# Kernel tuning notes

Hardware: AMD Instinct MI355X
Metric: run time of the kernel (lower is better)

## Reference

```python
import jax, jax.numpy as jnp
import numpy as np
from jax import lax

NB_VERTICES = 2048  # init kwarg nb_vertices
N_POINTS = 524288


def setup_inputs() -> dict:
    key = jax.random.key(0)
    pos = jax.random.normal(key, (N_POINTS, 3), dtype=jnp.float32)
    return {"pos": pos}


def _fps_indices(pos, m):
    """Single-pass iterative farthest point sampling.
    pos: [N, 3] float. Returns int32 indices [m].
    Maintains a running min squared-distance buffer (classic FPS).
    """
    N = pos.shape[0]
    big = jnp.asarray(jnp.finfo(pos.dtype).max, pos.dtype)
    min_d = jnp.full((N,), big, dtype=pos.dtype)
    idxs = jnp.zeros((m,), dtype=jnp.int32)  # idxs[0] = 0 (deterministic start)

    def body(i, carry):
        min_d, idxs = carry
        last = jnp.take(pos, idxs[i - 1], axis=0)          # [3]
        d = jnp.sum((pos - last[None, :]) ** 2, axis=-1)    # [N]
        min_d = jnp.minimum(min_d, d)
        nxt = jnp.argmax(min_d).astype(jnp.int32)
        idxs = idxs.at[i].set(nxt)
        return (min_d, idxs)

    _, idxs = lax.fori_loop(1, m, body, (min_d, idxs))
    return idxs


@jax.jit
def _forward(pos):
    # ratio = nb_vertices / N  ->  fps returns ceil(N*ratio) = nb_vertices
    # indices in a single pass, so the original while-loop runs once.
    idxs = _fps_indices(pos, NB_VERTICES)
    return pos[idxs]  # [nb_vertices, 3]


def reference(pos):
    return _forward(pos)
```

## Files before the change

kernel.cpp:

```cpp
#include <hip/hip_runtime.h>
#include <float.h>


#define NPTS     524288
#define MOUT     2048
#define NBLK     64
#define NTHR     512
#define NWAVE    (NTHR / 64)
#define GTHREADS (NBLK * NTHR)
#define PPT      (NPTS / GTHREADS)
#define SLOT_STRIDE 8
#define MASK51   ((1ull << 51) - 1)


__global__ void __launch_bounds__(NTHR, 1) fps_kernel(
    const float* __restrict__ pos, float* __restrict__ out,
    unsigned long long* __restrict__ slots)
{
    const unsigned tid  = threadIdx.x;
    const unsigned lane = tid & 63u;
    const unsigned wav  = tid >> 6;
    const unsigned blk  = blockIdx.x;
    const unsigned g    = blk * NTHR + tid;

    float X[PPT], Y[PPT], Z[PPT], D[PPT];
#pragma unroll
    for (int p = 0; p < PPT; ++p) {
        const unsigned idx = g + (unsigned)p * GTHREADS;
        X[p] = pos[3u * idx + 0];
        Y[p] = pos[3u * idx + 1];
        Z[p] = pos[3u * idx + 2];
        D[p] = FLT_MAX;
    }

    float px = pos[0], py = pos[1], pz = pos[2];
    if (g == 0) { out[0] = px; out[1] = py; out[2] = pz; }

    __shared__ unsigned long long sred[2][NWAVE];
    __shared__ unsigned long long sbc[2][4];
    if (tid < 4) { sbc[0][tid] = 0ull; sbc[1][tid] = 0ull; }

    for (int i = 1; i < MOUT; ++i) {
        float bv = -1.0f;
        unsigned bi = 0;
#pragma unroll
        for (int p = 0; p < PPT; ++p) {
            float dx = __fsub_rn(X[p], px);
            float dy = __fsub_rn(Y[p], py);
            float dz = __fsub_rn(Z[p], pz);
            float d  = __fadd_rn(__fadd_rn(__fmul_rn(dx, dx), __fmul_rn(dy, dy)),
                                 __fmul_rn(dz, dz));
            float m  = fminf(D[p], d);
            D[p] = m;
            if (m > bv) { bv = m; bi = g + (unsigned)p * GTHREADS; }
        }
        unsigned long long best =
            ((unsigned long long)__float_as_uint(bv) << 19) |
            (unsigned long long)((NPTS - 1u) - bi);

#pragma unroll
        for (int off = 32; off > 0; off >>= 1) {
            unsigned long long o = __shfl_xor(best, off, 64);
            if (o > best) best = o;
        }

        unsigned long long* sb = sred[i & 1];
        if (lane == 0) sb[wav] = best;
        __syncthreads();

        const unsigned long long tag = (unsigned long long)i;
        const unsigned long long tb  = tag << 51;

        if (wav == 0) {
            unsigned long long b2 = sb[lane & (NWAVE - 1u)];
#pragma unroll
            for (int off = NWAVE / 2; off > 0; off >>= 1) {
                unsigned long long o = __shfl_xor(b2, off, 64);
                if (o > b2) b2 = o;
            }

            unsigned long long* buf =
                slots + (unsigned)(i & 1) * (NBLK * SLOT_STRIDE);
            if (lane == 0) {
                __hip_atomic_store(&buf[blk * SLOT_STRIDE], tb | b2,
                                   __ATOMIC_RELAXED, __HIP_MEMORY_SCOPE_AGENT);
            }

            unsigned long long s;
            do {
                s = __hip_atomic_load(&buf[lane * SLOT_STRIDE],
                                      __ATOMIC_RELAXED, __HIP_MEMORY_SCOPE_AGENT);
                if ((s >> 51) == tag) break;
                __builtin_amdgcn_s_sleep(1);
            } while (true);
            unsigned long long c = s & MASK51;

            unsigned cidx = (NPTS - 1u) - (unsigned)(c & 0x7FFFFull);
            float cx = pos[3u * cidx + 0];
            float cy = pos[3u * cidx + 1];
            float cz = pos[3u * cidx + 2];

            unsigned long long win = c;
#pragma unroll
            for (int off = 32; off > 0; off >>= 1) {
                unsigned long long o = __shfl_xor(win, off, 64);
                if (o > win) win = o;
            }
            unsigned long long bal = __ballot(win == c);
            int src = __ffsll(bal) - 1;
            px = __shfl(cx, src, 64);
            py = __shfl(cy, src, 64);
            pz = __shfl(cz, src, 64);

            if (lane < 3) {
                float cv = (lane == 0) ? px : (lane == 1) ? py : pz;
                __hip_atomic_store(&sbc[i & 1][lane],
                                   tb | (unsigned long long)__float_as_uint(cv),
                                   __ATOMIC_RELAXED, __HIP_MEMORY_SCOPE_WORKGROUP);
            }

            if (blk == 0 && lane == 0) {
                out[3 * i + 0] = px; out[3 * i + 1] = py; out[3 * i + 2] = pz;
            }
        } else {
            unsigned long long xw, yw, zw;
            do {
                xw = __hip_atomic_load(&sbc[i & 1][0],
                                       __ATOMIC_RELAXED, __HIP_MEMORY_SCOPE_WORKGROUP);
                yw = __hip_atomic_load(&sbc[i & 1][1],
                                       __ATOMIC_RELAXED, __HIP_MEMORY_SCOPE_WORKGROUP);
                zw = __hip_atomic_load(&sbc[i & 1][2],
                                       __ATOMIC_RELAXED, __HIP_MEMORY_SCOPE_WORKGROUP);
                if (((xw >> 51) == tag) & ((yw >> 51) == tag) &
                    ((zw >> 51) == tag)) break;
                __builtin_amdgcn_s_sleep(1);
            } while (true);
            px = __uint_as_float((unsigned)xw);
            py = __uint_as_float((unsigned)yw);
            pz = __uint_as_float((unsigned)zw);
        }
    }
}

extern "C" void kernel_launch(void* const* d_in, const int* in_sizes, int n_in,
                              void* d_out, int out_size, void* d_ws, size_t ws_size,
                              hipStream_t stream) {
    const float* pos = (const float*)d_in[0];
    float* out = (float*)d_out;
    unsigned long long* slots = (unsigned long long*)d_ws;

    void* args[] = { (void*)&pos, (void*)&out, (void*)&slots };
    hipLaunchCooperativeKernel((void*)fps_kernel, dim3(NBLK), dim3(NTHR),
                               args, 0, stream);
}
```

Measured before the change: 5.165 ms.

## Carry winner coordinates through reductions and use DPP wave max

Each thread now tracks the coordinates of its best point. Those coordinates travel with the wave and block reductions and are published to the global slots alongside the packed key. This removes the dependent global gather of the winning point's position after the cross-block exchange, which sits on the serial critical path of every iteration. Shuffle-based 64-bit max reductions are replaced with DPP row operations plus readlane. In exchange there are more global stores and loads per slot, extra select instructions per point, and a multi-word tag protocol that relies on relaxed-ordering visibility.

```diff
diff --git a/kernel.cpp b/kernel.cpp
--- a/kernel.cpp
+++ b/kernel.cpp
@@ -13,6 +13,44 @@
 #define MASK51   ((1ull << 51) - 1)
 
 
+#define DPP_MAX_U64(v, ctrl) do {                                            \
+    unsigned _lo = (unsigned)__builtin_amdgcn_update_dpp(                    \
+        0, (int)(unsigned)(v), (ctrl), 0xf, 0xf, true);                      \
+    unsigned _hi = (unsigned)__builtin_amdgcn_update_dpp(                    \
+        0, (int)(unsigned)((v) >> 32), (ctrl), 0xf, 0xf, true);              \
+    unsigned long long _s = ((unsigned long long)_hi << 32) | _lo;           \
+    if (_s > (v)) (v) = _s;                                                  \
+} while (0)
+
+__device__ __forceinline__ unsigned long long wave_max_u64(unsigned long long v)
+{
+    DPP_MAX_U64(v, 0x111);
+    DPP_MAX_U64(v, 0x112);
+    DPP_MAX_U64(v, 0x114);
+    DPP_MAX_U64(v, 0x118);
+    DPP_MAX_U64(v, 0x142);
+    DPP_MAX_U64(v, 0x143);
+    unsigned lo = (unsigned)__builtin_amdgcn_readlane((int)(unsigned)v, 63);
+    unsigned hi = (unsigned)__builtin_amdgcn_readlane((int)(unsigned)(v >> 32), 63);
+    return ((unsigned long long)hi << 32) | lo;
+}
+
+__device__ __forceinline__ unsigned long long oct_max_u64(unsigned long long v)
+{
+    DPP_MAX_U64(v, 0x111);
+    DPP_MAX_U64(v, 0x112);
+    DPP_MAX_U64(v, 0x114);
+    unsigned lo = (unsigned)__builtin_amdgcn_readlane((int)(unsigned)v, 7);
+    unsigned hi = (unsigned)__builtin_amdgcn_readlane((int)(unsigned)(v >> 32), 7);
+    return ((unsigned long long)hi << 32) | lo;
+}
+
+__device__ __forceinline__ float readlane_f(float v, int l)
+{
+    return __uint_as_float(
+        (unsigned)__builtin_amdgcn_readlane((int)__float_as_uint(v), l));
+}
+
 __global__ void __launch_bounds__(NTHR, 1) fps_kernel(
     const float* __restrict__ pos, float* __restrict__ out,
     unsigned long long* __restrict__ slots)
@@ -37,6 +75,7 @@
     if (g == 0) { out[0] = px; out[1] = py; out[2] = pz; }
 
     __shared__ unsigned long long sred[2][NWAVE];
+    __shared__ float scx[2][NWAVE], scy[2][NWAVE], scz[2][NWAVE];
     __shared__ unsigned long long sbc[2][4];
     if (tid < 4) { sbc[0][tid] = 0ull; sbc[1][tid] = 0ull; }
 
@@ -54,18 +93,31 @@
             D[p] = m;
             if (m > bv) { bv = m; bi = g + (unsigned)p * GTHREADS; }
         }
-        unsigned long long best =
+
+        float bx = X[0], by = Y[0], bz = Z[0];
+#pragma unroll
+        for (int p = 1; p < PPT; ++p) {
+            const bool w = (bi == g + (unsigned)p * GTHREADS);
+            bx = w ? X[p] : bx;
+            by = w ? Y[p] : by;
+            bz = w ? Z[p] : bz;
+        }
+
+        const unsigned long long mine =
             ((unsigned long long)__float_as_uint(bv) << 19) |
             (unsigned long long)((NPTS - 1u) - bi);
 
-#pragma unroll
-        for (int off = 32; off > 0; off >>= 1) {
-            unsigned long long o = __shfl_xor(best, off, 64);
-            if (o > best) best = o;
-        }
+        const unsigned long long wbest = wave_max_u64(mine);
+        const int wsrc = __ffsll(__ballot(mine == wbest)) - 1;
+        const float wx = readlane_f(bx, wsrc);
+        const float wy = readlane_f(by, wsrc);
+        const float wz = readlane_f(bz, wsrc);
 
         unsigned long long* sb = sred[i & 1];
-        if (lane == 0) sb[wav] = best;
+        if (lane == 0) {
+            sb[wav] = wbest;
+            scx[i & 1][wav] = wx; scy[i & 1][wav] = wy; scz[i & 1][wav] = wz;
+        }
         __syncthreads();
 
         const unsigned long long tag = (unsigned long long)i;
@@ -73,44 +125,64 @@
 
         if (wav == 0) {
             unsigned long long b2 = sb[lane & (NWAVE - 1u)];
-#pragma unroll
-            for (int off = NWAVE / 2; off > 0; off >>= 1) {
-                unsigned long long o = __shfl_xor(b2, off, 64);
-                if (o > b2) b2 = o;
-            }
+            const unsigned long long bbest = oct_max_u64(b2);
+            const unsigned wavidx = (unsigned)(
+                __ffsll(__ballot((lane < 8u) & (b2 == bbest))) - 1);
 
             unsigned long long* buf =
                 slots + (unsigned)(i & 1) * (NBLK * SLOT_STRIDE);
             if (lane == 0) {
-                __hip_atomic_store(&buf[blk * SLOT_STRIDE], tb | b2,
+                const unsigned xb = __float_as_uint(scx[i & 1][wavidx]);
+                const unsigned yb = __float_as_uint(scy[i & 1][wavidx]);
+                const unsigned zb = __float_as_uint(scz[i & 1][wavidx]);
+                const unsigned long long w1 =
+                    tb | ((unsigned long long)xb << 19) |
+                    (unsigned long long)(yb & 0x7FFFFu);
+                const unsigned long long w2 =
+                    tb | ((unsigned long long)(yb >> 19) << 32) |
+                    (unsigned long long)zb;
+                unsigned long long* s0 = &buf[blk * SLOT_STRIDE];
+                __hip_atomic_store(s0 + 1, w1,
                                    __ATOMIC_RELAXED, __HIP_MEMORY_SCOPE_AGENT);
-            }
-
-            unsigned long long s;
+                __hip_atomic_store(s0 + 2, w2,
+                                   __ATOMIC_RELAXED, __HIP_MEMORY_SCOPE_AGENT);
+                __hip_atomic_store(s0 + 0, tb | bbest,
+                                   __ATOMIC_RELAXED, __HIP_MEMORY_SCOPE_AGENT);
+            }
+
+            unsigned long long* sl = &buf[lane * SLOT_STRIDE];
+            unsigned long long v0, v1, v2;
             do {
-                s = __hip_atomic_load(&buf[lane * SLOT_STRIDE],
-                                      __ATOMIC_RELAXED, __HIP_MEMORY_SCOPE_AGENT);
-                if ((s >> 51) == tag) break;
+                v0 = __hip_atomic_load(sl + 0, __ATOMIC_RELAXED,
+                                       __HIP_MEMORY_SCOPE_AGENT);
+                v1 = __hip_atomic_load(sl + 1, __ATOMIC_RELAXED,
+                                       __HIP_MEMORY_SCOPE_AGENT);
+                v2 = __hip_atomic_load(sl + 2, __ATOMIC_RELAXED,
+                                       __HIP_MEMORY_SCOPE_AGENT);
+                if ((v0 >> 51) == tag) break;
                 __builtin_amdgcn_s_sleep(1);
             } while (true);
-            unsigned long long c = s & MASK51;
-
-            unsigned cidx = (NPTS - 1u) - (unsigned)(c & 0x7FFFFull);
-            float cx = pos[3u * cidx + 0];
-            float cy = pos[3u * cidx + 1];
-            float cz = pos[3u * cidx + 2];
-
-            unsigned long long win = c;
-#pragma unroll
-            for (int off = 32; off > 0; off >>= 1) {
-                unsigned long long o = __shfl_xor(win, off, 64);
-                if (o > win) win = o;
-            }
-            unsigned long long bal = __ballot(win == c);
-            int src = __ffsll(bal) - 1;
-            px = __shfl(cx, src, 64);
-            py = __shfl(cy, src, 64);
-            pz = __shfl(cz, src, 64);
+            while (__ballot(((v1 >> 51) != tag) | ((v2 >> 51) != tag)) != 0ull) {
+                __builtin_amdgcn_s_sleep(1);
+                v1 = __hip_atomic_load(sl + 1, __ATOMIC_RELAXED,
+                                       __HIP_MEMORY_SCOPE_AGENT);
+                v2 = __hip_atomic_load(sl + 2, __ATOMIC_RELAXED,
+                                       __HIP_MEMORY_SCOPE_AGENT);
+            }
+
+            const unsigned long long c = v0 & MASK51;
+            const unsigned long long win = wave_max_u64(c);
+            const int src = __ffsll(__ballot(c == win)) - 1;
+            const unsigned xb = (unsigned)((v1 >> 19) & 0xFFFFFFFFull);
+            const unsigned yb = ((unsigned)((v2 >> 32) & 0x1FFFull) << 19) |
+                                (unsigned)(v1 & 0x7FFFFull);
+            const unsigned zb = (unsigned)(v2 & 0xFFFFFFFFull);
+            px = __uint_as_float(
+                (unsigned)__builtin_amdgcn_readlane((int)xb, src));
+            py = __uint_as_float(
+                (unsigned)__builtin_amdgcn_readlane((int)yb, src));
+            pz = __uint_as_float(
+                (unsigned)__builtin_amdgcn_readlane((int)zb, src));
 
             if (lane < 3) {
                 float cv = (lane == 0) ? px : (lane == 1) ? py : pz;
```

After: 5.893 ms. +14.1%, slower.

## Spread FPS over more blocks and use DPP reductions with release/acquire broadcast

Applied to the files above, without the earlier changes.

Changes the cooperative grid from 64x512 to 256x256 threads, so each block's wave 0 polls four slot entries per lane and combines them before a wave-level max. Shuffle-based 64-bit max reductions are replaced with DPP row and broadcast operations plus readlane. The in-block coordinate broadcast now uses a single release-tagged flag instead of three polled tags. The aim is to cut per-iteration reduction and sync latency in the serial 2047-step loop, at the cost of more blocks taking part in the grid-wide handshake.

```diff
diff --git a/kernel.cpp b/kernel.cpp
--- a/kernel.cpp
+++ b/kernel.cpp
@@ -4,14 +4,52 @@
 
 #define NPTS     524288
 #define MOUT     2048
-#define NBLK     64
-#define NTHR     512
+#define NBLK     256
+#define NTHR     256
 #define NWAVE    (NTHR / 64)
 #define GTHREADS (NBLK * NTHR)
 #define PPT      (NPTS / GTHREADS)
+#define NREG     4
 #define SLOT_STRIDE 8
 #define MASK51   ((1ull << 51) - 1)
 
+
+#define DPP_MAX_U64(v, ctrl) do {                                            \
+    unsigned _lo = (unsigned)__builtin_amdgcn_update_dpp(                    \
+        0, (int)(unsigned)(v), (ctrl), 0xf, 0xf, true);                      \
+    unsigned _hi = (unsigned)__builtin_amdgcn_update_dpp(                    \
+        0, (int)(unsigned)((v) >> 32), (ctrl), 0xf, 0xf, true);              \
+    unsigned long long _s = ((unsigned long long)_hi << 32) | _lo;           \
+    if (_s > (v)) (v) = _s;                                                  \
+} while (0)
+
+__device__ __forceinline__ unsigned long long wave_max_u64(unsigned long long v)
+{
+    DPP_MAX_U64(v, 0x111);
+    DPP_MAX_U64(v, 0x112);
+    DPP_MAX_U64(v, 0x114);
+    DPP_MAX_U64(v, 0x118);
+    DPP_MAX_U64(v, 0x142);
+    DPP_MAX_U64(v, 0x143);
+    unsigned lo = (unsigned)__builtin_amdgcn_readlane((int)(unsigned)v, 63);
+    unsigned hi = (unsigned)__builtin_amdgcn_readlane((int)(unsigned)(v >> 32), 63);
+    return ((unsigned long long)hi << 32) | lo;
+}
+
+__device__ __forceinline__ unsigned long long quad_max_u64(unsigned long long v)
+{
+    DPP_MAX_U64(v, 0x111);
+    DPP_MAX_U64(v, 0x112);
+    unsigned lo = (unsigned)__builtin_amdgcn_readlane((int)(unsigned)v, 3);
+    unsigned hi = (unsigned)__builtin_amdgcn_readlane((int)(unsigned)(v >> 32), 3);
+    return ((unsigned long long)hi << 32) | lo;
+}
+
+__device__ __forceinline__ float readlane_f(float v, int l)
+{
+    return __uint_as_float(
+        (unsigned)__builtin_amdgcn_readlane((int)__float_as_uint(v), l));
+}
 
 __global__ void __launch_bounds__(NTHR, 1) fps_kernel(
     const float* __restrict__ pos, float* __restrict__ out,
@@ -54,87 +92,85 @@
             D[p] = m;
             if (m > bv) { bv = m; bi = g + (unsigned)p * GTHREADS; }
         }
-        unsigned long long best =
+        const unsigned long long mine =
             ((unsigned long long)__float_as_uint(bv) << 19) |
             (unsigned long long)((NPTS - 1u) - bi);
 
-#pragma unroll
-        for (int off = 32; off > 0; off >>= 1) {
-            unsigned long long o = __shfl_xor(best, off, 64);
-            if (o > best) best = o;
-        }
-
-        unsigned long long* sb = sred[i & 1];
-        if (lane == 0) sb[wav] = best;
+        const unsigned long long wbest = wave_max_u64(mine);
+        if (lane == 0) sred[i & 1][wav] = wbest;
         __syncthreads();
 
         const unsigned long long tag = (unsigned long long)i;
         const unsigned long long tb  = tag << 51;
+        unsigned long long* buf = slots + (unsigned)(i & 1) * (NBLK * SLOT_STRIDE);
 
         if (wav == 0) {
-            unsigned long long b2 = sb[lane & (NWAVE - 1u)];
-#pragma unroll
-            for (int off = NWAVE / 2; off > 0; off >>= 1) {
-                unsigned long long o = __shfl_xor(b2, off, 64);
-                if (o > b2) b2 = o;
-            }
+            unsigned long long b2 = sred[i & 1][lane & (NWAVE - 1u)];
+            const unsigned long long bbest = quad_max_u64(b2);
 
-            unsigned long long* buf =
-                slots + (unsigned)(i & 1) * (NBLK * SLOT_STRIDE);
             if (lane == 0) {
-                __hip_atomic_store(&buf[blk * SLOT_STRIDE], tb | b2,
+                __hip_atomic_store(&buf[blk * SLOT_STRIDE], tb | bbest,
                                    __ATOMIC_RELAXED, __HIP_MEMORY_SCOPE_AGENT);
             }
 
-            unsigned long long s;
+            unsigned long long* base = buf + lane * SLOT_STRIDE;
+            unsigned long long s0, s1, s2, s3;
             do {
-                s = __hip_atomic_load(&buf[lane * SLOT_STRIDE],
-                                      __ATOMIC_RELAXED, __HIP_MEMORY_SCOPE_AGENT);
-                if ((s >> 51) == tag) break;
+                s0 = __hip_atomic_load(base + 0 * 64 * SLOT_STRIDE,
+                                       __ATOMIC_RELAXED, __HIP_MEMORY_SCOPE_AGENT);
+                s1 = __hip_atomic_load(base + 1 * 64 * SLOT_STRIDE,
+                                       __ATOMIC_RELAXED, __HIP_MEMORY_SCOPE_AGENT);
+                s2 = __hip_atomic_load(base + 2 * 64 * SLOT_STRIDE,
+                                       __ATOMIC_RELAXED, __HIP_MEMORY_SCOPE_AGENT);
+                s3 = __hip_atomic_load(base + 3 * 64 * SLOT_STRIDE,
+                                       __ATOMIC_RELAXED, __HIP_MEMORY_SCOPE_AGENT);
+                if (((s0 >> 51) == tag) & ((s1 >> 51) == tag) &
+                    ((s2 >> 51) == tag) & ((s3 >> 51) == tag)) break;
                 __builtin_amdgcn_s_sleep(1);
             } while (true);
-            unsigned long long c = s & MASK51;
 
-            unsigned cidx = (NPTS - 1u) - (unsigned)(c & 0x7FFFFull);
-            float cx = pos[3u * cidx + 0];
-            float cy = pos[3u * cidx + 1];
-            float cz = pos[3u * cidx + 2];
+            unsigned long long c0 = s0 & MASK51, c1 = s1 & MASK51;
+            unsigned long long c2 = s2 & MASK51, c3 = s3 & MASK51;
+            unsigned long long ca = (c0 > c1) ? c0 : c1;
+            unsigned long long cb = (c2 > c3) ? c2 : c3;
+            unsigned long long c  = (ca > cb) ? ca : cb;
 
-            unsigned long long win = c;
-#pragma unroll
-            for (int off = 32; off > 0; off >>= 1) {
-                unsigned long long o = __shfl_xor(win, off, 64);
-                if (o > win) win = o;
-            }
-            unsigned long long bal = __ballot(win == c);
-            int src = __ffsll(bal) - 1;
-            px = __shfl(cx, src, 64);
-            py = __shfl(cy, src, 64);
-            pz = __shfl(cz, src, 64);
+            const unsigned cidx = (NPTS - 1u) - (unsigned)(c & 0x7FFFFull);
+            const float cx = pos[3u * cidx + 0];
+            const float cy = pos[3u * cidx + 1];
+            const float cz = pos[3u * cidx + 2];
 
-            if (lane < 3) {
-                float cv = (lane == 0) ? px : (lane == 1) ? py : pz;
-                __hip_atomic_store(&sbc[i & 1][lane],
-                                   tb | (unsigned long long)__float_as_uint(cv),
+            const unsigned long long win = wave_max_u64(c);
+            const int src = __ffsll(__ballot(c == win)) - 1;
+            px = readlane_f(cx, src);
+            py = readlane_f(cy, src);
+            pz = readlane_f(cz, src);
+
+            if (lane == 0) {
+                __hip_atomic_store(&sbc[i & 1][1],
+                                   tb | (unsigned long long)__float_as_uint(py),
                                    __ATOMIC_RELAXED, __HIP_MEMORY_SCOPE_WORKGROUP);
+                __hip_atomic_store(&sbc[i & 1][2],
+                                   tb | (unsigned long long)__float_as_uint(pz),
+                                   __ATOMIC_RELAXED, __HIP_MEMORY_SCOPE_WORKGROUP);
+                __hip_atomic_store(&sbc[i & 1][0],
+                                   tb | (unsigned long long)__float_as_uint(px),
+                                   __ATOMIC_RELEASE, __HIP_MEMORY_SCOPE_WORKGROUP);
             }
 
             if (blk == 0 && lane == 0) {
                 out[3 * i + 0] = px; out[3 * i + 1] = py; out[3 * i + 2] = pz;
             }
         } else {
-            unsigned long long xw, yw, zw;
+            unsigned long long xw;
             do {
                 xw = __hip_atomic_load(&sbc[i & 1][0],
-                                       __ATOMIC_RELAXED, __HIP_MEMORY_SCOPE_WORKGROUP);
-                yw = __hip_atomic_load(&sbc[i & 1][1],
-                                       __ATOMIC_RELAXED, __HIP_MEMORY_SCOPE_WORKGROUP);
-                zw = __hip_atomic_load(&sbc[i & 1][2],
-                                       __ATOMIC_RELAXED, __HIP_MEMORY_SCOPE_WORKGROUP);
-                if (((xw >> 51) == tag) & ((yw >> 51) == tag) &
-                    ((zw >> 51) == tag)) break;
+                                       __ATOMIC_ACQUIRE, __HIP_MEMORY_SCOPE_WORKGROUP);
+                if ((xw >> 51) == tag) break;
                 __builtin_amdgcn_s_sleep(1);
             } while (true);
+            const unsigned long long yw = sbc[i & 1][1];
+            const unsigned long long zw = sbc[i & 1][2];
             px = __uint_as_float((unsigned)xw);
             py = __uint_as_float((unsigned)yw);
             pz = __uint_as_float((unsigned)zw);
```

Result: faster. 4.614 ms (-10.7%).
